# Kernel optimization log

Hardware: AMD Instinct MI355X
Metric: run time of the kernel (lower is better)

## Reference

```python
import jax, jax.numpy as jnp
import numpy as np

N_ATOMS = 1000
BOX_L = 30.0      # cubic cell edge (Angstrom)
MAX_CUTOFF = 8.0  # max(cutoff)


def _np_cart(a, b, c):
    # numpy equivalent of torch.cartesian_prod for 3 1-D arrays
    g = np.meshgrid(a, b, c, indexing='ij')
    return np.stack(g, axis=-1).reshape(-1, 3)


def _np_get_shifts(cell, cutoff):
    # mirrors TorchNeighborListRangeSeparated._get_shifts (pbc=True on all axes)
    recip = np.linalg.inv(cell).T
    inv_len = np.linalg.norm(recip, axis=1)
    nrep = np.ceil(cutoff * inv_len).astype(np.int64)
    r1 = np.arange(1, nrep[0] + 1, dtype=np.float64)
    r2 = np.arange(1, nrep[1] + 1, dtype=np.float64)
    r3 = np.arange(1, nrep[2] + 1, dtype=np.float64)
    o = np.zeros(1, dtype=np.float64)
    return np.concatenate([
        _np_cart(r1, r2, r3), _np_cart(r1, r2, o), _np_cart(r1, r2, -r3),
        _np_cart(r1, o, r3), _np_cart(r1, o, o), _np_cart(r1, o, -r3),
        _np_cart(r1, -r2, r3), _np_cart(r1, -r2, o), _np_cart(r1, -r2, -r3),
        _np_cart(o, r2, r3), _np_cart(o, r2, o), _np_cart(o, r2, -r3),
        _np_cart(o, o, r3)], axis=0)


def setup_inputs() -> dict:
    key = jax.random.key(0)
    cell_np = np.eye(3) * BOX_L
    shifts = jnp.asarray(_np_get_shifts(cell_np, MAX_CUTOFF), dtype=jnp.float32)  # [13,3]
    positions = jax.random.uniform(key, (N_ATOMS, 3), dtype=jnp.float32) * BOX_L
    return {
        "positions": positions,
        "cell": jnp.asarray(cell_np, dtype=jnp.float32),
        "shifts": shifts,
        "cutoffs": jnp.array([4.0, 8.0], dtype=jnp.float32),
    }


def reference(positions, cell, shifts, cutoffs):
    """PBC-aware pairwise distance^2 + per-cutoff neighbor masks.

    Returns:
      d2:    [P] squared distances over all candidate pairs
             (N*(N-1)/2 in-cell pairs followed by S*N*N shifted-image pairs)
      masks: [n_cutoffs, P] int32 in-cutoff indicator (d2 < cutoff^2)
    """
    n = positions.shape[0]
    # in-cell pairs (torch.combinations -> i<j)
    iu, ju = jnp.triu_indices(n, k=1)
    rij_c = positions[iu] - positions[ju]                       # [Pc,3]
    d2_c = jnp.sum(rij_c * rij_c, axis=-1)                      # [Pc]
    # shifted-image pairs: all (shift, i, j)
    shift_values = shifts @ cell                                # [S,3]
    rij_o = (positions[None, :, None, :] - positions[None, None, :, :]
             + shift_values[:, None, None, :])                  # [S,N,N,3]
    d2_o = jnp.sum(rij_o * rij_o, axis=-1).reshape(-1)          # [S*N*N]
    d2 = jnp.concatenate([d2_c, d2_o], axis=0)                  # [P]
    masks = (d2[None, :] < (cutoffs ** 2)[:, None]).astype(jnp.int32)
    return d2, masks
```

## Files before the change

### kernel.cpp

```cpp
#include <hip/hip_runtime.h>


__global__ void __launch_bounds__(256) tri_kernel(
    const float* __restrict__ pos,
    const float* __restrict__ cutoffs,
    int ncut, int n,
    float* __restrict__ out, long long P)
{
    int j = blockIdx.x * 256 + threadIdx.x;
    int i = blockIdx.y;
    if (j >= n || j <= i) return;

    double dx = (double)pos[3*i+0] - (double)pos[3*j+0];
    double dy = (double)pos[3*i+1] - (double)pos[3*j+1];
    double dz = (double)pos[3*i+2] - (double)pos[3*j+2];
    double d2 = dx*dx + dy*dy + dz*dz;

    long long off = (long long)i * (n - 1) - ((long long)i * (i - 1)) / 2 + (j - i - 1);
    out[off] = (float)d2;
    for (int c = 0; c < ncut; ++c) {
        double cv = (double)cutoffs[c];
        out[(long long)(c + 1) * P + off] = (d2 < cv * cv) ? 1.0f : 0.0f;
    }
}

__global__ void __launch_bounds__(256) shift_kernel(
    const float* __restrict__ pos,
    const float* __restrict__ cell,
    const float* __restrict__ shifts,
    const float* __restrict__ cutoffs,
    int ncut, int n,
    float* __restrict__ out, long long P, long long Pc)
{
    int i = blockIdx.y;
    int s = blockIdx.z;
    int jg = blockIdx.x * 256 + threadIdx.x;
    int j0 = jg << 2;
    if (j0 >= n) return;

    double s0 = (double)shifts[3*s+0], s1 = (double)shifts[3*s+1], s2 = (double)shifts[3*s+2];
    double sv0 = s0 * (double)cell[0] + s1 * (double)cell[3] + s2 * (double)cell[6];
    double sv1 = s0 * (double)cell[1] + s1 * (double)cell[4] + s2 * (double)cell[7];
    double sv2 = s0 * (double)cell[2] + s1 * (double)cell[5] + s2 * (double)cell[8];

    double pix = (double)pos[3*i+0];
    double piy = (double)pos[3*i+1];
    double piz = (double)pos[3*i+2];

    double cut2[4];
    for (int c = 0; c < ncut; ++c) { double cv = (double)cutoffs[c]; cut2[c] = cv * cv; }

    long long t0 = ((long long)s * n + i) * (long long)n + j0;

    if (j0 + 4 <= n) {
        const float4* pj = (const float4*)(pos + 3 * j0);
        float4 a = pj[0], b = pj[1], c4 = pj[2];
        float jx[4] = {a.x, a.w, b.z, c4.y};
        float jy[4] = {a.y, b.x, b.w, c4.z};
        float jz[4] = {a.z, b.y, c4.x, c4.w};

        float d2f[4];
        float mf[4][4];
        for (int k = 0; k < 4; ++k) {
            double dx = (pix - (double)jx[k]) + sv0;
            double dy = (piy - (double)jy[k]) + sv1;
            double dz = (piz - (double)jz[k]) + sv2;
            double d2 = dx*dx + dy*dy + dz*dz;
            d2f[k] = (float)d2;
            for (int c = 0; c < ncut; ++c) mf[c][k] = (d2 < cut2[c]) ? 1.0f : 0.0f;
        }
        *(float4*)(out + Pc + t0) = make_float4(d2f[0], d2f[1], d2f[2], d2f[3]);
        for (int c = 0; c < ncut; ++c)
            *(float4*)(out + (long long)(c + 1) * P + Pc + t0) =
                make_float4(mf[c][0], mf[c][1], mf[c][2], mf[c][3]);
    } else {
        for (int j = j0; j < n; ++j) {
            double dx = (pix - (double)pos[3*j+0]) + sv0;
            double dy = (piy - (double)pos[3*j+1]) + sv1;
            double dz = (piz - (double)pos[3*j+2]) + sv2;
            double d2 = dx*dx + dy*dy + dz*dz;
            long long t = t0 + (j - j0);
            out[Pc + t] = (float)d2;
            for (int c = 0; c < ncut; ++c)
                out[(long long)(c + 1) * P + Pc + t] = (d2 < cut2[c]) ? 1.0f : 0.0f;
        }
    }
}

extern "C" void kernel_launch(void* const* d_in, const int* in_sizes, int n_in,
                              void* d_out, int out_size, void* d_ws, size_t ws_size,
                              hipStream_t stream)
{
    const float* pos     = (const float*)d_in[0];
    const float* cell    = (const float*)d_in[1];
    const float* shifts  = (const float*)d_in[2];
    const float* cutoffs = (const float*)d_in[3];
    int n    = in_sizes[0] / 3;
    int S    = in_sizes[2] / 3;
    int ncut = in_sizes[3];

    long long Pc = (long long)n * (n - 1) / 2;
    long long P  = Pc + (long long)S * n * n;
    float* out = (float*)d_out;

    dim3 gt((n + 255) / 256, n, 1);
    tri_kernel<<<gt, dim3(256), 0, stream>>>(pos, cutoffs, ncut, n, out, P);

    int ngx = (((n + 3) / 4) + 255) / 256;
    dim3 gs(ngx, n, S);
    shift_kernel<<<gs, dim3(256), 0, stream>>>(pos, cell, shifts, cutoffs, ncut, n, out, P, Pc);
}
```

Measured before the change: 173.8 us.

## Fuse triangle and shifted-image kernels into one flat-indexed vectorized kernel

Replaces the two launches (a scalar in-cell triangle kernel and a per-row shifted-image kernel) with a single kernel over the flattened output index. Each thread writes four contiguous outputs with float4 stores. In-cell pairs recover (i,j) via a double-precision sqrt inversion of the triangular index, and shifted pairs recover (s,i,j) via integer division. This removes a launch, the idle threads of the triangle grid and its scalar stores, but adds index arithmetic (including a 64-bit divide) to every thread. A scalar fallback kernel covers sizes that are not multiples of four.

Result: no change. 170.9 us (-1.7%).

```diff
diff --git a/kernel.cpp b/kernel.cpp
--- a/kernel.cpp
+++ b/kernel.cpp
@@ -1,30 +1,8 @@
 #include <hip/hip_runtime.h>
+#include <math.h>
 
 
-__global__ void __launch_bounds__(256) tri_kernel(
-    const float* __restrict__ pos,
-    const float* __restrict__ cutoffs,
-    int ncut, int n,
-    float* __restrict__ out, long long P)
-{
-    int j = blockIdx.x * 256 + threadIdx.x;
-    int i = blockIdx.y;
-    if (j >= n || j <= i) return;
-
-    double dx = (double)pos[3*i+0] - (double)pos[3*j+0];
-    double dy = (double)pos[3*i+1] - (double)pos[3*j+1];
-    double dz = (double)pos[3*i+2] - (double)pos[3*j+2];
-    double d2 = dx*dx + dy*dy + dz*dz;
-
-    long long off = (long long)i * (n - 1) - ((long long)i * (i - 1)) / 2 + (j - i - 1);
-    out[off] = (float)d2;
-    for (int c = 0; c < ncut; ++c) {
-        double cv = (double)cutoffs[c];
-        out[(long long)(c + 1) * P + off] = (d2 < cv * cv) ? 1.0f : 0.0f;
-    }
-}
-
-__global__ void __launch_bounds__(256) shift_kernel(
+__global__ void __launch_bounds__(256) nbr_kernel(
     const float* __restrict__ pos,
     const float* __restrict__ cell,
     const float* __restrict__ shifts,
@@ -32,35 +10,38 @@
     int ncut, int n,
     float* __restrict__ out, long long P, long long Pc)
 {
-    int i = blockIdx.y;
-    int s = blockIdx.z;
-    int jg = blockIdx.x * 256 + threadIdx.x;
-    int j0 = jg << 2;
-    if (j0 >= n) return;
-
-    double s0 = (double)shifts[3*s+0], s1 = (double)shifts[3*s+1], s2 = (double)shifts[3*s+2];
-    double sv0 = s0 * (double)cell[0] + s1 * (double)cell[3] + s2 * (double)cell[6];
-    double sv1 = s0 * (double)cell[1] + s1 * (double)cell[4] + s2 * (double)cell[7];
-    double sv2 = s0 * (double)cell[2] + s1 * (double)cell[5] + s2 * (double)cell[8];
-
-    double pix = (double)pos[3*i+0];
-    double piy = (double)pos[3*i+1];
-    double piz = (double)pos[3*i+2];
+    long long p0 = ((long long)blockIdx.x * 256 + threadIdx.x) << 2;
+    if (p0 >= P) return;
 
     double cut2[4];
     for (int c = 0; c < ncut; ++c) { double cv = (double)cutoffs[c]; cut2[c] = cv * cv; }
 
-    long long t0 = ((long long)s * n + i) * (long long)n + j0;
+    float d2f[4];
+    float mf[4][4];
 
-    if (j0 + 4 <= n) {
+    if (p0 >= Pc) {
+        long long q = p0 - Pc;
+        unsigned nn = (unsigned)n * (unsigned)n;
+        unsigned s  = (unsigned)((unsigned long long)q / nn);
+        unsigned r  = (unsigned)((unsigned long long)q - (unsigned long long)s * nn);
+        unsigned i  = r / (unsigned)n;
+        unsigned j0 = r - i * (unsigned)n;
+
+        double s0 = (double)shifts[3*s+0], s1 = (double)shifts[3*s+1], s2 = (double)shifts[3*s+2];
+        double sv0 = s0 * (double)cell[0] + s1 * (double)cell[3] + s2 * (double)cell[6];
+        double sv1 = s0 * (double)cell[1] + s1 * (double)cell[4] + s2 * (double)cell[7];
+        double sv2 = s0 * (double)cell[2] + s1 * (double)cell[5] + s2 * (double)cell[8];
+
+        double pix = (double)pos[3*i+0];
+        double piy = (double)pos[3*i+1];
+        double piz = (double)pos[3*i+2];
+
         const float4* pj = (const float4*)(pos + 3 * j0);
         float4 a = pj[0], b = pj[1], c4 = pj[2];
         float jx[4] = {a.x, a.w, b.z, c4.y};
         float jy[4] = {a.y, b.x, b.w, c4.z};
         float jz[4] = {a.z, b.y, c4.x, c4.w};
 
-        float d2f[4];
-        float mf[4][4];
         for (int k = 0; k < 4; ++k) {
             double dx = (pix - (double)jx[k]) + sv0;
             double dy = (piy - (double)jy[k]) + sv1;
@@ -69,22 +50,80 @@
             d2f[k] = (float)d2;
             for (int c = 0; c < ncut; ++c) mf[c][k] = (d2 < cut2[c]) ? 1.0f : 0.0f;
         }
-        *(float4*)(out + Pc + t0) = make_float4(d2f[0], d2f[1], d2f[2], d2f[3]);
-        for (int c = 0; c < ncut; ++c)
-            *(float4*)(out + (long long)(c + 1) * P + Pc + t0) =
-                make_float4(mf[c][0], mf[c][1], mf[c][2], mf[c][3]);
     } else {
-        for (int j = j0; j < n; ++j) {
-            double dx = (pix - (double)pos[3*j+0]) + sv0;
-            double dy = (piy - (double)pos[3*j+1]) + sv1;
-            double dz = (piz - (double)pos[3*j+2]) + sv2;
+        long long tn = 2LL * n - 1;
+        for (int k = 0; k < 4; ++k) {
+            long long p = p0 + k;
+            double D = (double)(tn * tn) - 8.0 * (double)p;
+            long long i = (long long)(((double)tn - sqrt(D)) * 0.5);
+            if (i < 0) i = 0;
+            if (i > n - 2) i = n - 2;
+            while ((i + 1) * (tn - (i + 1)) / 2 <= p) ++i;
+            while (i * (tn - i) / 2 > p) --i;
+            long long j = p - i * (tn - i) / 2 + i + 1;
+
+            double dx = (double)pos[3*i+0] - (double)pos[3*j+0];
+            double dy = (double)pos[3*i+1] - (double)pos[3*j+1];
+            double dz = (double)pos[3*i+2] - (double)pos[3*j+2];
             double d2 = dx*dx + dy*dy + dz*dz;
-            long long t = t0 + (j - j0);
-            out[Pc + t] = (float)d2;
-            for (int c = 0; c < ncut; ++c)
-                out[(long long)(c + 1) * P + Pc + t] = (d2 < cut2[c]) ? 1.0f : 0.0f;
+            d2f[k] = (float)d2;
+            for (int c = 0; c < ncut; ++c) mf[c][k] = (d2 < cut2[c]) ? 1.0f : 0.0f;
         }
     }
+
+    *(float4*)(out + p0) = make_float4(d2f[0], d2f[1], d2f[2], d2f[3]);
+    for (int c = 0; c < ncut; ++c)
+        *(float4*)(out + (long long)(c + 1) * P + p0) =
+            make_float4(mf[c][0], mf[c][1], mf[c][2], mf[c][3]);
+}
+
+__global__ void __launch_bounds__(256) nbr_kernel_scalar(
+    const float* __restrict__ pos,
+    const float* __restrict__ cell,
+    const float* __restrict__ shifts,
+    const float* __restrict__ cutoffs,
+    int ncut, int n,
+    float* __restrict__ out, long long P, long long Pc)
+{
+    long long p = (long long)blockIdx.x * 256 + threadIdx.x;
+    if (p >= P) return;
+
+    double cut2[4];
+    for (int c = 0; c < ncut; ++c) { double cv = (double)cutoffs[c]; cut2[c] = cv * cv; }
+
+    double d2;
+    if (p >= Pc) {
+        long long q = p - Pc;
+        unsigned long long nn = (unsigned long long)n * n;
+        unsigned s = (unsigned)(q / nn);
+        unsigned long long r = q - (unsigned long long)s * nn;
+        unsigned i = (unsigned)(r / n);
+        unsigned j = (unsigned)(r - (unsigned long long)i * n);
+        double s0 = (double)shifts[3*s+0], s1 = (double)shifts[3*s+1], s2 = (double)shifts[3*s+2];
+        double sv0 = s0*(double)cell[0] + s1*(double)cell[3] + s2*(double)cell[6];
+        double sv1 = s0*(double)cell[1] + s1*(double)cell[4] + s2*(double)cell[7];
+        double sv2 = s0*(double)cell[2] + s1*(double)cell[5] + s2*(double)cell[8];
+        double dx = ((double)pos[3*i+0] - (double)pos[3*j+0]) + sv0;
+        double dy = ((double)pos[3*i+1] - (double)pos[3*j+1]) + sv1;
+        double dz = ((double)pos[3*i+2] - (double)pos[3*j+2]) + sv2;
+        d2 = dx*dx + dy*dy + dz*dz;
+    } else {
+        long long tn = 2LL * n - 1;
+        double D = (double)(tn * tn) - 8.0 * (double)p;
+        long long i = (long long)(((double)tn - sqrt(D)) * 0.5);
+        if (i < 0) i = 0;
+        if (i > n - 2) i = n - 2;
+        while ((i + 1) * (tn - (i + 1)) / 2 <= p) ++i;
+        while (i * (tn - i) / 2 > p) --i;
+        long long j = p - i * (tn - i) / 2 + i + 1;
+        double dx = (double)pos[3*i+0] - (double)pos[3*j+0];
+        double dy = (double)pos[3*i+1] - (double)pos[3*j+1];
+        double dz = (double)pos[3*i+2] - (double)pos[3*j+2];
+        d2 = dx*dx + dy*dy + dz*dz;
+    }
+    out[p] = (float)d2;
+    for (int c = 0; c < ncut; ++c)
+        out[(long long)(c + 1) * P + p] = (d2 < cut2[c]) ? 1.0f : 0.0f;
 }
 
 extern "C" void kernel_launch(void* const* d_in, const int* in_sizes, int n_in,
@@ -103,10 +142,14 @@
     long long P  = Pc + (long long)S * n * n;
     float* out = (float*)d_out;
 
-    dim3 gt((n + 255) / 256, n, 1);
-    tri_kernel<<<gt, dim3(256), 0, stream>>>(pos, cutoffs, ncut, n, out, P);
-
-    int ngx = (((n + 3) / 4) + 255) / 256;
-    dim3 gs(ngx, n, S);
-    shift_kernel<<<gs, dim3(256), 0, stream>>>(pos, cell, shifts, cutoffs, ncut, n, out, P, Pc);
+    if ((n & 3) == 0) {
+        long long chunks = P >> 2;
+        int blocks = (int)((chunks + 255) / 256);
+        nbr_kernel<<<blocks, 256, 0, stream>>>(pos, cell, shifts, cutoffs,
+                                               ncut, n, out, P, Pc);
+    } else {
+        int blocks = (int)((P + 255) / 256);
+        nbr_kernel_scalar<<<blocks, 256, 0, stream>>>(pos, cell, shifts, cutoffs,
+                                                      ncut, n, out, P, Pc);
+    }
 }
```
